# Performance work log

Hardware: AMD Instinct MI355X
Metric: run time of the kernel (lower is better)

Reference implementation:

```python
import jax, jax.numpy as jnp
import numpy as np

V, E, N, H, L = 50257, 768, 1024, 12, 6
HD = E // H
FF = 4 * E
B = 2


def sinusoidal_pos(n, dim):
    # Faithful to populate_sinusoidal_pos_emb: interleaved sin/cos with the
    # torch code's (slightly nonstandard) cos exponent 2*arange(1,dim,2)/dim.
    pos = jnp.arange(n, dtype=jnp.float32)[:, None]
    i = jnp.arange(0, dim, 2, dtype=jnp.float32)
    j = jnp.arange(1, dim, 2, dtype=jnp.float32)
    s = jnp.sin(pos / jnp.power(10000.0, 2.0 * i / dim))  # [n, dim/2]
    c = jnp.cos(pos / jnp.power(10000.0, 2.0 * j / dim))  # [n, dim/2]
    return jnp.stack([s, c], axis=-1).reshape(n, dim)


def gelu(x):
    # tanh-approximation GELU (custom gelu.GELU in the repo)
    return 0.5 * x * (1.0 + jnp.tanh(jnp.sqrt(2.0 / jnp.pi) * (x + 0.044715 * x * x * x)))


def layer_norm(x, g, b, eps=1e-5):
    mu = jnp.mean(x, axis=-1, keepdims=True)
    var = jnp.var(x, axis=-1, keepdims=True)  # biased, matches unbiased=False
    return g * (x - mu) / jnp.sqrt(var + eps) + b


def setup_inputs() -> dict:
    key = jax.random.key(0)
    ks = jax.random.split(key, 12)
    s = 0.02
    inp = {
        "x": jax.random.randint(ks[0], (B, N), 0, V),
        "tok_emb": s * jax.random.normal(ks[1], (V, E), dtype=jnp.float32),
        "wq": s * jax.random.normal(ks[2], (L, E, E), dtype=jnp.float32),
        "wk": s * jax.random.normal(ks[3], (L, E, E), dtype=jnp.float32),
        "wv": s * jax.random.normal(ks[4], (L, E, E), dtype=jnp.float32),
        "wo": s * jax.random.normal(ks[5], (L, E, E), dtype=jnp.float32),
        "bo": jnp.zeros((L, E), dtype=jnp.float32),
        "ln1_g": jnp.ones((L, E), dtype=jnp.float32),
        "ln1_b": jnp.zeros((L, E), dtype=jnp.float32),
        "ln2_g": jnp.ones((L, E), dtype=jnp.float32),
        "ln2_b": jnp.zeros((L, E), dtype=jnp.float32),
        "w1": s * jax.random.normal(ks[6], (L, E, FF), dtype=jnp.float32),
        "b1": jnp.zeros((L, FF), dtype=jnp.float32),
        "w2": s * jax.random.normal(ks[7], (L, FF, E), dtype=jnp.float32),
        "b2": jnp.zeros((L, E), dtype=jnp.float32),
        "lnf_g": jnp.ones((E,), dtype=jnp.float32),
        "lnf_b": jnp.zeros((E,), dtype=jnp.float32),
        "w_head": s * jax.random.normal(ks[8], (E, V), dtype=jnp.float32),
    }
    return inp


def reference(x, tok_emb, wq, wk, wv, wo, bo, ln1_g, ln1_b, ln2_g, ln2_b,
              w1, b1, w2, b2, lnf_g, lnf_b, w_head):
    b, n = x.shape
    h = tok_emb[x] + sinusoidal_pos(n, E)  # [B, N, E]; dropout is identity (p=0)
    causal = jnp.triu(jnp.ones((n, n), dtype=bool), k=1)  # True above diagonal
    scale = HD ** 0.5
    for l in range(L):
        # attention sub-block
        y = layer_norm(h, ln1_g[l], ln1_b[l])
        q = (y @ wq[l]).reshape(b, n, H, HD).transpose(0, 2, 1, 3)  # [B,H,N,HD]
        k = (y @ wk[l]).reshape(b, n, H, HD).transpose(0, 2, 1, 3)
        v = (y @ wv[l]).reshape(b, n, H, HD).transpose(0, 2, 1, 3)
        attn = jnp.einsum('bhqd,bhkd->bhqk', q, k)  # [B,H,N,N]
        attn = jnp.where(causal, -jnp.inf, attn) / scale  # mask before scale, as in source
        attn = jax.nn.softmax(attn, axis=-1)
        o = jnp.einsum('bhqk,bhkd->bhqd', attn, v)
        o = o.transpose(0, 2, 1, 3).reshape(b, n, E) @ wo[l] + bo[l]
        h = h + o
        # FFN sub-block
        y = layer_norm(h, ln2_g[l], ln2_b[l])
        y = gelu(y @ w1[l] + b1[l]) @ w2[l] + b2[l]
        h = h + y
    h = layer_norm(h, lnf_g, lnf_b)
    return h @ w_head  # [B, N, V]
```

## Files before the change

### kernel.cpp

```cpp
#include <hip/hip_runtime.h>
#include <hip/hip_bf16.h>
#include <math.h>

#define B_  2
#define N_  1024
#define E_  768
#define H_  12
#define HD_ 64
#define L_  6
#define FF_ 3072
#define V_  50257
#define VPAD_ 50304
#define QKVW_ 2304
#define M_  (B_ * N_)

#define OFF_QKV_ 0
#define OFF_WO_  (QKVW_ * E_)
#define OFF_W1_  (OFF_WO_ + E_ * E_)
#define OFF_W2_  (OFF_W1_ + FF_ * E_)
#define WSLAB_   ((size_t)(OFF_W2_ + E_ * FF_))

typedef short short8 __attribute__((ext_vector_type(8)));
typedef float f32x4 __attribute__((ext_vector_type(4)));

__device__ __forceinline__ float gelu_f(float x) {
  return 0.5f * x * (1.0f + tanhf(0.7978845608028654f * (x + 0.044715f * x * x * x)));
}

__device__ __forceinline__ unsigned short f2bf(float f) {
  __hip_bfloat16 b = __float2bfloat16(f);
  return *reinterpret_cast<unsigned short*>(&b);
}

__device__ __forceinline__ void async_ld16(const void* g, void* l) {
  __builtin_amdgcn_global_load_lds(
      (const __attribute__((address_space(1))) void*)g,
      (__attribute__((address_space(3))) void*)l, 16, 0, 0);
}

__global__ __launch_bounds__(256) void embed_kernel(const int* __restrict__ x,
    const float* __restrict__ tok, float* __restrict__ h) {
  int idx = blockIdx.x * 256 + threadIdx.x;
  const int total = B_ * N_ * E_;
  if (idx >= total) return;
  int e  = idx % E_;
  int bn = idx / E_;
  int n  = bn % N_;
  int t  = x[bn];
  float freq = expf(-9.210340371976184f * (float)(2 * e) / (float)E_);
  float arg  = (float)n * freq;
  float pe   = (e & 1) ? cosf(arg) : sinf(arg);
  h[idx] = tok[(size_t)t * E_ + e] + pe;
}

__global__ __launch_bounds__(256) void layernorm_kernel(const float* __restrict__ in,
    __hip_bfloat16* __restrict__ out, const float* __restrict__ g, const float* __restrict__ b) {
  int row = blockIdx.x;
  const float* xr = in + (size_t)row * E_;
  __shared__ float red[256];
  int tid = threadIdx.x;
  float s = 0.f, ss = 0.f;
  for (int e = tid; e < E_; e += 256) { float v = xr[e]; s += v; ss += v * v; }
  red[tid] = s; __syncthreads();
  for (int o = 128; o > 0; o >>= 1) { if (tid < o) red[tid] += red[tid + o]; __syncthreads(); }
  float mean = red[0] / (float)E_;
  __syncthreads();
  red[tid] = ss; __syncthreads();
  for (int o = 128; o > 0; o >>= 1) { if (tid < o) red[tid] += red[tid + o]; __syncthreads(); }
  float var = red[0] / (float)E_ - mean * mean;
  float inv = rsqrtf(var + 1e-5f);
  for (int e = tid; e < E_; e += 256)
    out[(size_t)row * E_ + e] = __float2bfloat16(g[e] * (xr[e] - mean) * inv + b[e]);
}

__global__ __launch_bounds__(256) void transpose_cast_kernel(const float* __restrict__ in,
    __hip_bfloat16* __restrict__ out, int K, int Nn) {
  __shared__ float t[64][65];
  int k0 = blockIdx.x * 64, n0 = blockIdx.y * 64;
  int tid = threadIdx.x;
  int c = tid & 63, rg = tid >> 6;
#pragma unroll
  for (int i = 0; i < 16; ++i) {
    int r = rg * 16 + i;
    int n = n0 + c;
    t[r][c] = (n < Nn) ? in[(size_t)(k0 + r) * Nn + n] : 0.0f;
  }
  __syncthreads();
#pragma unroll
  for (int i = 0; i < 16; ++i) {
    int ro = rg * 16 + i;
    out[(size_t)(n0 + ro) * K + (k0 + c)] = __float2bfloat16(t[c][ro]);
  }
}

__global__ __launch_bounds__(256) void wtrans_kernel(
    const float* __restrict__ wq, const float* __restrict__ wk,
    const float* __restrict__ wv, const float* __restrict__ wo,
    const float* __restrict__ w1, const float* __restrict__ w2,
    __hip_bfloat16* __restrict__ out, int l0) {
  int bid = blockIdx.x;
  int lay = bid / 1728;
  int t = bid - lay * 1728;
  int lsrc = l0 + lay;
  __hip_bfloat16* ob = out + (size_t)lay * WSLAB_;
  const float* src; __hip_bfloat16* dst;
  int K, Nn, ntk;
  if (t < 576) {
    int which = t / 144; t -= which * 144;
    K = E_; Nn = E_; ntk = 12;
    if (which == 0)      { src = wq + (size_t)lsrc * E_ * E_; dst = ob + OFF_QKV_; }
    else if (which == 1) { src = wk + (size_t)lsrc * E_ * E_; dst = ob + OFF_QKV_ + (size_t)E_ * E_; }
    else if (which == 2) { src = wv + (size_t)lsrc * E_ * E_; dst = ob + OFF_QKV_ + (size_t)2 * E_ * E_; }
    else                 { src = wo + (size_t)lsrc * E_ * E_; dst = ob + OFF_WO_; }
  } else if (t < 1152) {
    t -= 576; K = E_; Nn = FF_; ntk = 12;
    src = w1 + (size_t)lsrc * E_ * FF_; dst = ob + OFF_W1_;
  } else {
    t -= 1152; K = FF_; Nn = E_; ntk = 48;
    src = w2 + (size_t)lsrc * FF_ * E_; dst = ob + OFF_W2_;
  }
  int kt = t % ntk, nt = t / ntk;
  int k0 = kt * 64, n0 = nt * 64;
  __shared__ float tt[64][65];
  int tid = threadIdx.x;
  int c = tid & 63, rg = tid >> 6;
#pragma unroll
  for (int i = 0; i < 16; ++i) {
    int r = rg * 16 + i;
    tt[r][c] = src[(size_t)(k0 + r) * Nn + n0 + c];
  }
  __syncthreads();
#pragma unroll
  for (int i = 0; i < 16; ++i) {
    int ro = rg * 16 + i;
    dst[(size_t)(n0 + ro) * K + (k0 + c)] = __float2bfloat16(tt[c][ro]);
  }
}

template<int BM>
__global__ __launch_bounds__(256) void gemm_bt_kernel(
    const __hip_bfloat16* __restrict__ A, const __hip_bfloat16* __restrict__ Bt,
    const float* __restrict__ bias, const float* __restrict__ R,
    float* __restrict__ Cf, __hip_bfloat16* __restrict__ Cb,
    __hip_bfloat16* __restrict__ vt,
    int Nn, int K, int flags) {
  constexpr int NROWS = BM + 64;
  constexpr int WRT = BM / 4;
  constexpr int MF  = WRT / 16;
  __shared__ __align__(16) unsigned short SM[2 * NROWS * 64];
  int tid = threadIdx.x;
  int w = tid >> 6, l = tid & 63;
  int bx = blockIdx.x, by = blockIdx.y;
  int row0 = by * BM, col0 = bx * 64;
  int lr = l & 15, kg = l >> 4;
  const unsigned short* Ag = (const unsigned short*)A;
  const unsigned short* Bg = (const unsigned short*)Bt;
  int srow = l >> 3;
  int schunk = (l & 7) ^ srow;

  constexpr int NS = NROWS / 32;
  constexpr int A8 = BM / 8;
  auto stage = [&](int buf, int k0) {
    unsigned short* As = SM + buf * (NROWS * 64);
    unsigned short* Bs = As + BM * 64;
#pragma unroll
    for (int s = 0; s < NS; ++s) {
      int idx8 = s * 4 + w;
      if (idx8 < A8)
        async_ld16(Ag + (size_t)(row0 + idx8 * 8 + srow) * K + k0 + schunk * 8,
                   &As[idx8 * 8 * 64]);
      else
        async_ld16(Bg + (size_t)(col0 + (idx8 - A8) * 8 + srow) * K + k0 + schunk * 8,
                   &Bs[(idx8 - A8) * 8 * 64]);
    }
  };

  f32x4 acc[MF][4];
#pragma unroll
  for (int m = 0; m < MF; ++m)
#pragma unroll
    for (int n = 0; n < 4; ++n) acc[m][n] = (f32x4){0.f, 0.f, 0.f, 0.f};

  int nt = K >> 6;
  stage(0, 0);
  __syncthreads();
  int cur = 0;
  for (int t = 0; t < nt; ++t) {
    if (t + 1 < nt) stage(cur ^ 1, (t + 1) << 6);
    const unsigned short* As = SM + cur * (NROWS * 64);
    const unsigned short* Bs = As + BM * 64;
#pragma unroll
    for (int hf = 0; hf < 2; ++hf) {
      short8 af[MF], bf[4];
#pragma unroll
      for (int m = 0; m < MF; ++m) {
        int r = w * WRT + m * 16 + lr;
        af[m] = *(const short8*)&As[r * 64 + ((((hf << 2) | kg)) ^ (lr & 7)) * 8];
      }
#pragma unroll
      for (int n = 0; n < 4; ++n) {
        int r = n * 16 + lr;
        bf[n] = *(const short8*)&Bs[r * 64 + ((((hf << 2) | kg)) ^ (lr & 7)) * 8];
      }
#pragma unroll
      for (int m = 0; m < MF; ++m)
#pragma unroll
        for (int n = 0; n < 4; ++n)
          acc[m][n] = __builtin_amdgcn_mfma_f32_16x16x32_bf16(af[m], bf[n], acc[m][n], 0, 0, 0);
    }
    if (t + 1 < nt) { __syncthreads(); cur ^= 1; }
  }

  unsigned short* vtb = (unsigned short*)vt;
#pragma unroll
  for (int n = 0; n < 4; ++n) {
    int col = col0 + n * 16 + lr;
    if (col >= Nn) continue;
    float bv = bias ? bias[col] : 0.f;
    bool to_vt = (vtb != nullptr) && (col >= 2 * E_);
    int hh = 0, dd = 0;
    if (to_vt) { int c2 = col - 2 * E_; hh = c2 >> 6; dd = c2 & 63; }
#pragma unroll
    for (int m = 0; m < MF; ++m) {
#pragma unroll
      for (int j = 0; j < 4; ++j) {
        int row = row0 + w * WRT + m * 16 + kg * 4 + j;
        float val = acc[m][n][j] + bv;
        if (flags & 1) val = gelu_f(val);
        if (R) val += R[(size_t)row * Nn + col];
        if (Cf) Cf[(size_t)row * Nn + col] = val;
        if (to_vt) {
          int bz = row >> 10, nn = row & (N_ - 1);
          vtb[((size_t)(bz * H_ + hh) * HD_ + dd) * N_ + nn] = f2bf(val);
        } else if (Cb) {
          Cb[(size_t)row * Nn + col] = __float2bfloat16(val);
        }
      }
    }
  }
}

__global__ __launch_bounds__(256) void head_gemm_kernel(
    const __hip_bfloat16* __restrict__ A, const __hip_bfloat16* __restrict__ Bt,
    float* __restrict__ Cf, int Nn, int K, int nrt) {
  __shared__ __align__(16) unsigned short SM[2 * 256 * 32];
  int tid = threadIdx.x;
  int w = tid >> 6, l = tid & 63;
  int wr = w >> 1, wc = w & 1;
  int bid = blockIdx.x;
  int q = gridDim.x >> 3;
  int nb = (bid & 7) * q + (bid >> 3);
  int bx = nb / nrt, by = nb - bx * nrt;
  int row0 = by * 128, col0 = bx * 128;
  int lr = l & 15, kg = l >> 4;
  const unsigned short* Ag = (const unsigned short*)A;
  const unsigned short* Bg = (const unsigned short*)Bt;
  int srow = l >> 2;
  int schunk = (l & 3) ^ (l >> 4);

  auto stage = [&](int buf, int k0) {
    unsigned short* As = SM + buf * (256 * 32);
    unsigned short* Bs = As + 128 * 32;
#pragma unroll
    for (int s = 0; s < 4; ++s) {
      int g = s * 4 + w;
      if (g < 8)
        async_ld16(Ag + (size_t)(row0 + g * 16 + srow) * K + k0 + schunk * 8,
                   &As[g * 16 * 32]);
      else
        async_ld16(Bg + (size_t)(col0 + (g - 8) * 16 + srow) * K + k0 + schunk * 8,
                   &Bs[(g - 8) * 16 * 32]);
    }
  };

  f32x4 acc[4][4];
#pragma unroll
  for (int m = 0; m < 4; ++m)
#pragma unroll
    for (int n = 0; n < 4; ++n) acc[m][n] = (f32x4){0.f, 0.f, 0.f, 0.f};

  int rchunk = (kg ^ ((lr >> 2) & 3)) * 8;
  int nt = K >> 5;
  stage(0, 0);
  __syncthreads();
  int cur = 0;
  for (int t = 0; t < nt; ++t) {
    if (t + 1 < nt) stage(cur ^ 1, (t + 1) << 5);
    const unsigned short* As = SM + cur * (256 * 32);
    const unsigned short* Bs = As + 128 * 32;
    short8 af[4], bf[4];
#pragma unroll
    for (int m = 0; m < 4; ++m)
      af[m] = *(const short8*)&As[(wr * 64 + m * 16 + lr) * 32 + rchunk];
#pragma unroll
    for (int n = 0; n < 4; ++n)
      bf[n] = *(const short8*)&Bs[(wc * 64 + n * 16 + lr) * 32 + rchunk];
#pragma unroll
    for (int m = 0; m < 4; ++m)
#pragma unroll
      for (int n = 0; n < 4; ++n)
        acc[m][n] = __builtin_amdgcn_mfma_f32_16x16x32_bf16(af[m], bf[n], acc[m][n], 0, 0, 0);
    if (t + 1 < nt) { __syncthreads(); cur ^= 1; }
  }

  float* Ls = (float*)SM;
  bool nfull = (col0 + 128 <= Nn);
#pragma unroll
  for (int p = 0; p < 4; ++p) {
    __syncthreads();
    if (wr == (p >> 1)) {
      int mb = (p & 1) * 2;
#pragma unroll
      for (int m2 = 0; m2 < 2; ++m2)
#pragma unroll
        for (int n = 0; n < 4; ++n)
#pragma unroll
          for (int j = 0; j < 4; ++j)
            Ls[(m2 * 16 + kg * 4 + j) * 128 + ((wc * 64 + n * 16 + lr) ^ (16 * (kg & 1)))]
                = acc[mb + m2][n][j];
    }
    __syncthreads();
    int rbase = row0 + p * 32;
    if (nfull) {
#pragma unroll
      for (int i = 0; i < 16; ++i) {
        int idx = i * 256 + tid;
        int r = idx >> 7, c = idx & 127;
        float v = Ls[r * 128 + (c ^ (16 * ((r >> 2) & 1)))];
        __builtin_nontemporal_store(v, &Cf[(size_t)(rbase + r) * Nn + col0 + c]);
      }
    } else {
      for (int i = 0; i < 16; ++i) {
        int idx = i * 256 + tid;
        int r = idx >> 7, c = idx & 127;
        if (col0 + c < Nn) {
          float v = Ls[r * 128 + (c ^ (16 * ((r >> 2) & 1)))];
          __builtin_nontemporal_store(v, &Cf[(size_t)(rbase + r) * Nn + col0 + c]);
        }
      }
    }
  }
}

#define PRS_ 40
__global__ __launch_bounds__(64) void fattn_kernel(
    const __hip_bfloat16* __restrict__ qkv, const __hip_bfloat16* __restrict__ vt,
    __hip_bfloat16* __restrict__ o) {
  int qt = blockIdx.x, hh = blockIdx.y, bz = blockIdx.z;
  int q0 = qt * 16;
  int l = threadIdx.x;
  int lr = l & 15, kg = l >> 4;
  const unsigned short* base = (const unsigned short*)qkv;
  const unsigned short* vtb = (const unsigned short*)vt + ((size_t)(bz * H_ + hh)) * HD_ * N_;
  __shared__ __align__(16) unsigned short P[16 * PRS_];

  short8 qf[2];
  const unsigned short* qrow = base + (size_t)(bz * N_ + q0 + lr) * QKVW_ + hh * HD_;
#pragma unroll
  for (int c = 0; c < 2; ++c) qf[c] = *(const short8*)(qrow + c * 32 + kg * 8);

  float mrow[4], lsum[4];
  f32x4 accO[4];
#pragma unroll
  for (int j = 0; j < 4; ++j) { mrow[j] = -INFINITY; lsum[j] = 0.f; }
#pragma unroll
  for (int db = 0; db < 4; ++db) accO[db] = (f32x4){0.f, 0.f, 0.f, 0.f};

  int nsteps = (q0 + 16 + 31) / 32;
  for (int kt = 0; kt < nsteps; ++kt) {
    f32x4 s[2];
#pragma unroll
    for (int t = 0; t < 2; ++t) {
      const unsigned short* krow = base + (size_t)(bz * N_ + kt * 32 + t * 16 + lr) * QKVW_ + E_ + hh * HD_;
      short8 kf0 = *(const short8*)(krow + kg * 8);
      short8 kf1 = *(const short8*)(krow + 32 + kg * 8);
      f32x4 acc = (f32x4){0.f, 0.f, 0.f, 0.f};
      acc = __builtin_amdgcn_mfma_f32_16x16x32_bf16(qf[0], kf0, acc, 0, 0, 0);
      acc = __builtin_amdgcn_mfma_f32_16x16x32_bf16(qf[1], kf1, acc, 0, 0, 0);
      s[t] = acc;
    }
    float pm[2][4];
#pragma unroll
    for (int t = 0; t < 2; ++t) {
      int kglob = kt * 32 + t * 16 + lr;
#pragma unroll
      for (int j = 0; j < 4; ++j) {
        int qglob = q0 + kg * 4 + j;
        pm[t][j] = (kglob <= qglob) ? s[t][j] * 0.125f : -INFINITY;
      }
    }
#pragma unroll
    for (int j = 0; j < 4; ++j) {
      float tm = fmaxf(pm[0][j], pm[1][j]);
      tm = fmaxf(tm, __shfl_xor(tm, 1));
      tm = fmaxf(tm, __shfl_xor(tm, 2));
      tm = fmaxf(tm, __shfl_xor(tm, 4));
      tm = fmaxf(tm, __shfl_xor(tm, 8));
      float mnew = fmaxf(mrow[j], tm);
      float alpha = __expf(mrow[j] - mnew);
      float p0 = __expf(pm[0][j] - mnew);
      float p1 = __expf(pm[1][j] - mnew);
      float rs = p0 + p1;
      rs += __shfl_xor(rs, 1);
      rs += __shfl_xor(rs, 2);
      rs += __shfl_xor(rs, 4);
      rs += __shfl_xor(rs, 8);
      lsum[j] = lsum[j] * alpha + rs;
      mrow[j] = mnew;
#pragma unroll
      for (int db = 0; db < 4; ++db) accO[db][j] *= alpha;
      P[(kg * 4 + j) * PRS_ + lr]      = f2bf(p0);
      P[(kg * 4 + j) * PRS_ + 16 + lr] = f2bf(p1);
    }
    __syncthreads();
    short8 pa = *(const short8*)&P[lr * PRS_ + kg * 8];
#pragma unroll
    for (int db = 0; db < 4; ++db) {
      short8 vf = *(const short8*)(vtb + (size_t)(db * 16 + lr) * N_ + kt * 32 + kg * 8);
      accO[db] = __builtin_amdgcn_mfma_f32_16x16x32_bf16(pa, vf, accO[db], 0, 0, 0);
    }
    __syncthreads();
  }
  unsigned short* ob = (unsigned short*)o;
#pragma unroll
  for (int j = 0; j < 4; ++j) {
    float inv = 1.f / lsum[j];
    size_t orow = (size_t)(bz * N_ + q0 + kg * 4 + j) * E_ + hh * HD_;
#pragma unroll
    for (int db = 0; db < 4; ++db)
      ob[orow + db * 16 + lr] = f2bf(accO[db][j] * inv);
  }
}

extern "C" void kernel_launch(void* const* d_in, const int* in_sizes, int n_in,
                              void* d_out, int out_size, void* d_ws, size_t ws_size,
                              hipStream_t stream) {
  const int*   x     = (const int*)  d_in[0];
  const float* tok   = (const float*)d_in[1];
  const float* wq    = (const float*)d_in[2];
  const float* wk    = (const float*)d_in[3];
  const float* wv    = (const float*)d_in[4];
  const float* wo    = (const float*)d_in[5];
  const float* bo    = (const float*)d_in[6];
  const float* ln1g  = (const float*)d_in[7];
  const float* ln1b  = (const float*)d_in[8];
  const float* ln2g  = (const float*)d_in[9];
  const float* ln2b  = (const float*)d_in[10];
  const float* w1    = (const float*)d_in[11];
  const float* b1    = (const float*)d_in[12];
  const float* w2    = (const float*)d_in[13];
  const float* b2    = (const float*)d_in[14];
  const float* lnfg  = (const float*)d_in[15];
  const float* lnfb  = (const float*)d_in[16];
  const float* whead = (const float*)d_in[17];
  float* out = (float*)d_out;

  char* wsb = (char*)d_ws;
  size_t off = 0;
  auto alloc = [&](size_t bytes) -> void* {
    void* p = wsb + off; off += (bytes + 255) & ~(size_t)255; return p;
  };
  float*           h        = (float*)          alloc((size_t)M_ * E_ * 4);
  __hip_bfloat16*  y_bf     = (__hip_bfloat16*) alloc((size_t)M_ * E_ * 2);
  __hip_bfloat16*  qkv_bf   = (__hip_bfloat16*) alloc((size_t)M_ * QKVW_ * 2);
  __hip_bfloat16*  vt_bf    = (__hip_bfloat16*) alloc((size_t)B_ * H_ * HD_ * N_ * 2);
  __hip_bfloat16*  o_bf     = (__hip_bfloat16*) alloc((size_t)M_ * E_ * 2);
  __hip_bfloat16*  mid_bf   = (__hip_bfloat16*) alloc((size_t)M_ * FF_ * 2);
  __hip_bfloat16*  whead_bt = (__hip_bfloat16*) alloc((size_t)VPAD_ * E_ * 2);
  bool preall = (off + (size_t)6 * WSLAB_ * 2 <= ws_size);
  __hip_bfloat16* wslab = (__hip_bfloat16*) alloc(((size_t)(preall ? 6 : 1)) * WSLAB_ * 2);

  dim3 blk(256);

  embed_kernel<<<(B_ * N_ * E_ + 255) / 256, blk, 0, stream>>>(x, tok, h);
  transpose_cast_kernel<<<dim3(E_ / 64, VPAD_ / 64), blk, 0, stream>>>(whead, whead_bt, E_, V_);
  if (preall)
    wtrans_kernel<<<6 * 1728, blk, 0, stream>>>(wq, wk, wv, wo, w1, w2, wslab, 0);

  dim3 gqkv(QKVW_ / 64, M_ / 128);
  dim3 gffn1(FF_ / 64, M_ / 128);
  dim3 gsm(E_ / 64, M_ / 64);
  dim3 gfa(N_ / 16, H_, B_);

  for (int l = 0; l < L_; ++l) {
    if (!preall)
      wtrans_kernel<<<1728, blk, 0, stream>>>(wq, wk, wv, wo, w1, w2, wslab, l);
    __hip_bfloat16* wb = wslab + (preall ? (size_t)l * WSLAB_ : 0);

    layernorm_kernel<<<M_, blk, 0, stream>>>(h, y_bf, ln1g + (size_t)l * E_, ln1b + (size_t)l * E_);
    gemm_bt_kernel<128><<<gqkv, blk, 0, stream>>>(y_bf, wb + OFF_QKV_, nullptr, nullptr,
        nullptr, qkv_bf, vt_bf, QKVW_, E_, 0);
    fattn_kernel<<<gfa, dim3(64), 0, stream>>>(qkv_bf, vt_bf, o_bf);
    gemm_bt_kernel<64><<<gsm, blk, 0, stream>>>(o_bf, wb + OFF_WO_, bo + (size_t)l * E_, h,
        h, nullptr, nullptr, E_, E_, 0);
    layernorm_kernel<<<M_, blk, 0, stream>>>(h, y_bf, ln2g + (size_t)l * E_, ln2b + (size_t)l * E_);
    gemm_bt_kernel<128><<<gffn1, blk, 0, stream>>>(y_bf, wb + OFF_W1_, b1 + (size_t)l * FF_,
        nullptr, nullptr, mid_bf, nullptr, FF_, E_, 1);
    gemm_bt_kernel<64><<<gsm, blk, 0, stream>>>(mid_bf, wb + OFF_W2_, b2 + (size_t)l * E_, h,
        h, nullptr, nullptr, E_, FF_, 0);
  }

  layernorm_kernel<<<M_, blk, 0, stream>>>(h, y_bf, lnfg, lnfb);
  head_gemm_kernel<<<dim3((VPAD_ / 128) * (M_ / 128)), blk, 0, stream>>>(
      y_bf, whead_bt, out, V_, E_, M_ / 128);
}
```

Measured before the change: 1.337 ms.

## Process 32 query rows per attention block and retune head GEMM LDS swizzle

The flash attention kernel now handles two 16-row query groups per wavefront, so each loaded K tile and V fragment is reused across 32 queries and the grid is halved. This cuts global K/V load traffic and per-block overhead, at the cost of more registers and fewer blocks. The head GEMM's LDS XOR swizzle pattern is also changed on both the store and read side to reduce bank conflicts.

```diff
diff --git a/kernel.cpp b/kernel.cpp
--- a/kernel.cpp
+++ b/kernel.cpp
@@ -256,7 +256,7 @@
   const unsigned short* Ag = (const unsigned short*)A;
   const unsigned short* Bg = (const unsigned short*)Bt;
   int srow = l >> 2;
-  int schunk = (l & 3) ^ (l >> 4);
+  int schunk = (l & 3) ^ ((l >> 3) & 3);
 
   auto stage = [&](int buf, int k0) {
     unsigned short* As = SM + buf * (256 * 32);
@@ -279,7 +279,7 @@
 #pragma unroll
     for (int n = 0; n < 4; ++n) acc[m][n] = (f32x4){0.f, 0.f, 0.f, 0.f};
 
-  int rchunk = (kg ^ ((lr >> 2) & 3)) * 8;
+  int rchunk = (kg ^ ((lr >> 1) & 3)) * 8;
   int nt = K >> 5;
   stage(0, 0);
   __syncthreads();
@@ -347,89 +347,111 @@
     const __hip_bfloat16* __restrict__ qkv, const __hip_bfloat16* __restrict__ vt,
     __hip_bfloat16* __restrict__ o) {
   int qt = blockIdx.x, hh = blockIdx.y, bz = blockIdx.z;
-  int q0 = qt * 16;
+  int q0 = qt * 32;
   int l = threadIdx.x;
   int lr = l & 15, kg = l >> 4;
   const unsigned short* base = (const unsigned short*)qkv;
   const unsigned short* vtb = (const unsigned short*)vt + ((size_t)(bz * H_ + hh)) * HD_ * N_;
-  __shared__ __align__(16) unsigned short P[16 * PRS_];
-
-  short8 qf[2];
-  const unsigned short* qrow = base + (size_t)(bz * N_ + q0 + lr) * QKVW_ + hh * HD_;
-#pragma unroll
-  for (int c = 0; c < 2; ++c) qf[c] = *(const short8*)(qrow + c * 32 + kg * 8);
-
-  float mrow[4], lsum[4];
-  f32x4 accO[4];
-#pragma unroll
-  for (int j = 0; j < 4; ++j) { mrow[j] = -INFINITY; lsum[j] = 0.f; }
-#pragma unroll
-  for (int db = 0; db < 4; ++db) accO[db] = (f32x4){0.f, 0.f, 0.f, 0.f};
-
-  int nsteps = (q0 + 16 + 31) / 32;
+  __shared__ __align__(16) unsigned short P[32 * PRS_];
+
+  short8 qf[2][2];
+#pragma unroll
+  for (int g = 0; g < 2; ++g) {
+    const unsigned short* qrow = base + (size_t)(bz * N_ + q0 + g * 16 + lr) * QKVW_ + hh * HD_;
+#pragma unroll
+    for (int c = 0; c < 2; ++c) qf[g][c] = *(const short8*)(qrow + c * 32 + kg * 8);
+  }
+
+  float mrow[2][4], lsum[2][4];
+  f32x4 accO[2][4];
+#pragma unroll
+  for (int g = 0; g < 2; ++g)
+#pragma unroll
+    for (int j = 0; j < 4; ++j) { mrow[g][j] = -INFINITY; lsum[g][j] = 0.f; }
+#pragma unroll
+  for (int g = 0; g < 2; ++g)
+#pragma unroll
+    for (int db = 0; db < 4; ++db) accO[g][db] = (f32x4){0.f, 0.f, 0.f, 0.f};
+
+  int nsteps = qt + 1;
   for (int kt = 0; kt < nsteps; ++kt) {
-    f32x4 s[2];
+    short8 kf[2][2];
 #pragma unroll
     for (int t = 0; t < 2; ++t) {
       const unsigned short* krow = base + (size_t)(bz * N_ + kt * 32 + t * 16 + lr) * QKVW_ + E_ + hh * HD_;
-      short8 kf0 = *(const short8*)(krow + kg * 8);
-      short8 kf1 = *(const short8*)(krow + 32 + kg * 8);
-      f32x4 acc = (f32x4){0.f, 0.f, 0.f, 0.f};
-      acc = __builtin_amdgcn_mfma_f32_16x16x32_bf16(qf[0], kf0, acc, 0, 0, 0);
-      acc = __builtin_amdgcn_mfma_f32_16x16x32_bf16(qf[1], kf1, acc, 0, 0, 0);
-      s[t] = acc;
-    }
-    float pm[2][4];
-#pragma unroll
-    for (int t = 0; t < 2; ++t) {
-      int kglob = kt * 32 + t * 16 + lr;
+      kf[t][0] = *(const short8*)(krow + kg * 8);
+      kf[t][1] = *(const short8*)(krow + 32 + kg * 8);
+    }
+    f32x4 s[2][2];
+#pragma unroll
+    for (int g = 0; g < 2; ++g)
+#pragma unroll
+      for (int t = 0; t < 2; ++t) {
+        f32x4 acc = (f32x4){0.f, 0.f, 0.f, 0.f};
+        acc = __builtin_amdgcn_mfma_f32_16x16x32_bf16(qf[g][0], kf[t][0], acc, 0, 0, 0);
+        acc = __builtin_amdgcn_mfma_f32_16x16x32_bf16(qf[g][1], kf[t][1], acc, 0, 0, 0);
+        s[g][t] = acc;
+      }
+#pragma unroll
+    for (int g = 0; g < 2; ++g) {
+      float pm[2][4];
+#pragma unroll
+      for (int t = 0; t < 2; ++t) {
+        int kglob = kt * 32 + t * 16 + lr;
+#pragma unroll
+        for (int j = 0; j < 4; ++j) {
+          int qglob = q0 + g * 16 + kg * 4 + j;
+          pm[t][j] = (kglob <= qglob) ? s[g][t][j] * 0.125f : -INFINITY;
+        }
+      }
 #pragma unroll
       for (int j = 0; j < 4; ++j) {
-        int qglob = q0 + kg * 4 + j;
-        pm[t][j] = (kglob <= qglob) ? s[t][j] * 0.125f : -INFINITY;
-      }
-    }
-#pragma unroll
-    for (int j = 0; j < 4; ++j) {
-      float tm = fmaxf(pm[0][j], pm[1][j]);
-      tm = fmaxf(tm, __shfl_xor(tm, 1));
-      tm = fmaxf(tm, __shfl_xor(tm, 2));
-      tm = fmaxf(tm, __shfl_xor(tm, 4));
-      tm = fmaxf(tm, __shfl_xor(tm, 8));
-      float mnew = fmaxf(mrow[j], tm);
-      float alpha = __expf(mrow[j] - mnew);
-      float p0 = __expf(pm[0][j] - mnew);
-      float p1 = __expf(pm[1][j] - mnew);
-      float rs = p0 + p1;
-      rs += __shfl_xor(rs, 1);
-      rs += __shfl_xor(rs, 2);
-      rs += __shfl_xor(rs, 4);
-      rs += __shfl_xor(rs, 8);
-      lsum[j] = lsum[j] * alpha + rs;
-      mrow[j] = mnew;
-#pragma unroll
-      for (int db = 0; db < 4; ++db) accO[db][j] *= alpha;
-      P[(kg * 4 + j) * PRS_ + lr]      = f2bf(p0);
-      P[(kg * 4 + j) * PRS_ + 16 + lr] = f2bf(p1);
+        float tm = fmaxf(pm[0][j], pm[1][j]);
+        tm = fmaxf(tm, __shfl_xor(tm, 1));
+        tm = fmaxf(tm, __shfl_xor(tm, 2));
+        tm = fmaxf(tm, __shfl_xor(tm, 4));
+        tm = fmaxf(tm, __shfl_xor(tm, 8));
+        float mnew = fmaxf(mrow[g][j], tm);
+        float alpha = __expf(mrow[g][j] - mnew);
+        float p0 = __expf(pm[0][j] - mnew);
+        float p1 = __expf(pm[1][j] - mnew);
+        float rs = p0 + p1;
+        rs += __shfl_xor(rs, 1);
+        rs += __shfl_xor(rs, 2);
+        rs += __shfl_xor(rs, 4);
+        rs += __shfl_xor(rs, 8);
+        lsum[g][j] = lsum[g][j] * alpha + rs;
+        mrow[g][j] = mnew;
+#pragma unroll
+        for (int db = 0; db < 4; ++db) accO[g][db][j] *= alpha;
+        P[(g * 16 + kg * 4 + j) * PRS_ + lr]      = f2bf(p0);
+        P[(g * 16 + kg * 4 + j) * PRS_ + 16 + lr] = f2bf(p1);
+      }
     }
     __syncthreads();
-    short8 pa = *(const short8*)&P[lr * PRS_ + kg * 8];
+    short8 pa[2];
+#pragma unroll
+    for (int g = 0; g < 2; ++g)
+      pa[g] = *(const short8*)&P[(g * 16 + lr) * PRS_ + kg * 8];
 #pragma unroll
     for (int db = 0; db < 4; ++db) {
       short8 vf = *(const short8*)(vtb + (size_t)(db * 16 + lr) * N_ + kt * 32 + kg * 8);
-      accO[db] = __builtin_amdgcn_mfma_f32_16x16x32_bf16(pa, vf, accO[db], 0, 0, 0);
+      accO[0][db] = __builtin_amdgcn_mfma_f32_16x16x32_bf16(pa[0], vf, accO[0][db], 0, 0, 0);
+      accO[1][db] = __builtin_amdgcn_mfma_f32_16x16x32_bf16(pa[1], vf, accO[1][db], 0, 0, 0);
     }
     __syncthreads();
   }
   unsigned short* ob = (unsigned short*)o;
 #pragma unroll
-  for (int j = 0; j < 4; ++j) {
-    float inv = 1.f / lsum[j];
-    size_t orow = (size_t)(bz * N_ + q0 + kg * 4 + j) * E_ + hh * HD_;
-#pragma unroll
-    for (int db = 0; db < 4; ++db)
-      ob[orow + db * 16 + lr] = f2bf(accO[db][j] * inv);
-  }
+  for (int g = 0; g < 2; ++g)
+#pragma unroll
+    for (int j = 0; j < 4; ++j) {
+      float inv = 1.f / lsum[g][j];
+      size_t orow = (size_t)(bz * N_ + q0 + g * 16 + kg * 4 + j) * E_ + hh * HD_;
+#pragma unroll
+      for (int db = 0; db < 4; ++db)
+        ob[orow + db * 16 + lr] = f2bf(accO[g][db][j] * inv);
+    }
 }
 
 extern "C" void kernel_launch(void* const* d_in, const int* in_sizes, int n_in,
@@ -480,7 +502,7 @@
   dim3 gqkv(QKVW_ / 64, M_ / 128);
   dim3 gffn1(FF_ / 64, M_ / 128);
   dim3 gsm(E_ / 64, M_ / 64);
-  dim3 gfa(N_ / 16, H_, B_);
+  dim3 gfa(N_ / 32, H_, B_);
 
   for (int l = 0; l < L_; ++l) {
     if (!preall)
```

Result: slower. 1.414 ms (+5.7%).
